# Kernel tuning notes

Measured on AMD Instinct MI355X. Metric: run time of the kernel, lower is better.

## Reference

```python
import jax, jax.numpy as jnp
import numpy as np

H = 512          # HIDDEN_DIM
W = 480          # WINDOWWIDTH
NL = 8           # NUMLABELS (output_dim)
STEPS = W // 15  # 32 decoder steps
ATT = W // 16    # 30 attention positions
B = 4            # window batch
L = 12           # per-frame sequence length
D_IN = 32        # input_dim
N = B * W        # 1920 frame sequences


def _lstm(x, Wih, Whh, bih, bhh):
    # x: [T, Bn, Din] -> per-step hidden/cell states [T, Bn, Hd] (torch LSTM gate order i,f,g,o)
    xp = x @ Wih.T + (bih + bhh)
    h0 = jnp.zeros((x.shape[1], Whh.shape[1]), x.dtype)
    def step(carry, xt):
        h, c = carry
        g = xt + h @ Whh.T
        i, f, gg, o = jnp.split(g, 4, axis=-1)
        c = jax.nn.sigmoid(f) * c + jax.nn.sigmoid(i) * jnp.tanh(gg)
        h = jax.nn.sigmoid(o) * jnp.tanh(c)
        return (h, c), (h, c)
    _, (hs, cs) = jax.lax.scan(step, (h0, h0), xp)
    return hs, cs


def _bilstm(x, Wf, Uf, bf, cf, Wb, Ub, bb, cb):
    # x: [Bt, T, D] batch_first; returns ([Bt, T, 2H], h_fwd_final, h_bwd_final)
    xt = jnp.swapaxes(x, 0, 1)
    hf, _ = _lstm(xt, Wf, Uf, bf, cf)
    hb, _ = _lstm(xt[::-1], Wb, Ub, bb, cb)
    out = jnp.concatenate([hf, hb[::-1]], axis=-1)
    return jnp.swapaxes(out, 0, 1), hf[-1], hb[-1]


def _forward(xs, xlengths, enc_Wih, enc_Whh, enc_bih, enc_bhh,
             penc_Wih_f, penc_Whh_f, penc_bih_f, penc_bhh_f,
             penc_Wih_b, penc_Whh_b, penc_bih_b, penc_bhh_b,
             attn_W, attn_b, comb_W, comb_b,
             gru_Wih, gru_Whh, gru_bih, gru_bhh, out_W, out_b):
    # frame-level encoder: packed sequences -> (h, c) at each sequence's true length
    hs, cs = _lstm(xs, enc_Wih, enc_Whh, enc_bih, enc_bhh)   # [L, N, H] each
    idx = xlengths - 1
    ar = jnp.arange(N)
    ctx = jnp.concatenate([hs[idx, ar], cs[idx, ar]], axis=-1)  # [N, 2H]
    ctx = ctx.reshape(B, W // 2, 4 * H)
    # pyramidal BiLSTM stack (dropout is identity at eval)
    out = ctx
    hf = hb = None
    for i in range(4):
        out, hf, hb = _bilstm(ctx, penc_Wih_f[i], penc_Whh_f[i], penc_bih_f[i], penc_bhh_f[i],
                              penc_Wih_b[i], penc_Whh_b[i], penc_bih_b[i], penc_bhh_b[i])
        if i < 3:
            ctx = out.reshape(B, W // (2 ** (i + 2)), 4 * H)
    enc_out = out                                   # [B, ATT, 2H]
    hidden0 = jnp.concatenate([hf, hb], axis=-1)    # [B, 2H]

    def dstep(carry, _):
        inp, h = carry                              # [B, NL], [B, 2H]
        aw = jax.nn.softmax(jnp.concatenate([inp, h], axis=-1) @ attn_W.T + attn_b, axis=-1)
        ctxv = jnp.einsum('bt,btd->bd', aw, enc_out)
        x = jax.nn.relu(jnp.concatenate([inp, ctxv], axis=-1) @ comb_W.T + comb_b)
        # torch GRU cell (gate order r, z, n)
        gi = x @ gru_Wih.T + gru_bih
        gh = h @ gru_Whh.T + gru_bhh
        ir, iz, inn = jnp.split(gi, 3, axis=-1)
        hr, hz, hn = jnp.split(gh, 3, axis=-1)
        r = jax.nn.sigmoid(ir + hr)
        z = jax.nn.sigmoid(iz + hz)
        n = jnp.tanh(inn + r * hn)
        hnew = (1.0 - z) * n + z * h
        logp = jax.nn.log_softmax(hnew @ out_W.T + out_b, axis=-1)
        return (logp, hnew), logp                   # free-running: next input = log-probs

    inp0 = jnp.zeros((B, NL), xs.dtype)
    _, outs = jax.lax.scan(dstep, (inp0, hidden0), None, length=STEPS)  # [STEPS, B, NL]
    return jnp.swapaxes(outs, 0, 1).reshape(B * STEPS, NL)


def setup_inputs() -> dict:
    key = jax.random.key(0)
    ks = jax.random.split(key, 24)
    s = 0.03
    def nrm(k, shape):
        return jax.random.normal(k, shape, dtype=jnp.float32) * s
    return {
        'xs': jax.random.normal(ks[0], (L, N, D_IN), dtype=jnp.float32),
        'xlengths': jax.random.randint(ks[1], (N,), 1, L + 1, dtype=jnp.int32),
        'enc_Wih': nrm(ks[2], (4 * H, D_IN)),
        'enc_Whh': nrm(ks[3], (4 * H, H)),
        'enc_bih': nrm(ks[4], (4 * H,)),
        'enc_bhh': nrm(ks[5], (4 * H,)),
        'penc_Wih_f': nrm(ks[6], (4, 4 * H, 4 * H)),
        'penc_Whh_f': nrm(ks[7], (4, 4 * H, H)),
        'penc_bih_f': nrm(ks[8], (4, 4 * H)),
        'penc_bhh_f': nrm(ks[9], (4, 4 * H)),
        'penc_Wih_b': nrm(ks[10], (4, 4 * H, 4 * H)),
        'penc_Whh_b': nrm(ks[11], (4, 4 * H, H)),
        'penc_bih_b': nrm(ks[12], (4, 4 * H)),
        'penc_bhh_b': nrm(ks[13], (4, 4 * H)),
        'attn_W': nrm(ks[14], (ATT, 2 * H + NL)),
        'attn_b': nrm(ks[15], (ATT,)),
        'comb_W': nrm(ks[16], (H, 2 * H + NL)),
        'comb_b': nrm(ks[17], (H,)),
        'gru_Wih': nrm(ks[18], (3 * 2 * H, H)),
        'gru_Whh': nrm(ks[19], (3 * 2 * H, 2 * H)),
        'gru_bih': nrm(ks[20], (3 * 2 * H,)),
        'gru_bhh': nrm(ks[21], (3 * 2 * H,)),
        'out_W': nrm(ks[22], (NL, 2 * H)),
        'out_b': nrm(ks[23], (NL,)),
    }


def reference(xs, xlengths, enc_Wih, enc_Whh, enc_bih, enc_bhh,
              penc_Wih_f, penc_Whh_f, penc_bih_f, penc_bhh_f,
              penc_Wih_b, penc_Whh_b, penc_bih_b, penc_bhh_b,
              attn_W, attn_b, comb_W, comb_b,
              gru_Wih, gru_Whh, gru_bih, gru_bhh, out_W, out_b):
    return _forward(xs, xlengths, enc_Wih, enc_Whh, enc_bih, enc_bhh,
                    penc_Wih_f, penc_Whh_f, penc_bih_f, penc_bhh_f,
                    penc_Wih_b, penc_Whh_b, penc_bih_b, penc_bhh_b,
                    attn_W, attn_b, comb_W, comb_b,
                    gru_Wih, gru_Whh, gru_bih, gru_bhh, out_W, out_b)
```

## Files before the change

kernel.cpp:

```cpp
#include <hip/hip_runtime.h>
#include <stdint.h>

typedef __attribute__((ext_vector_type(8))) __bf16 bf16x8;
typedef __attribute__((ext_vector_type(4))) float f32x4;
typedef __attribute__((ext_vector_type(4))) unsigned u32x4;

#define DEVI static __device__ __forceinline__
#define SENT 0xFFFFFFFFu

DEVI bf16x8 bzero8(){ bf16x8 r;
#pragma unroll
  for (int i=0;i<8;++i) r[i]=(__bf16)0.0f; return r; }

DEVI bf16x8 ld8(const __bf16* p){ return *(const bf16x8*)p; }
DEVI void st8(__bf16* p, bf16x8 v){ *(bf16x8*)p = v; }

DEVI f32x4 MFMA(bf16x8 a, bf16x8 b, f32x4 c){
  return __builtin_amdgcn_mfma_f32_16x16x32_bf16(a, b, c, 0, 0, 0);
}

DEVI float sigf(float x){ return 1.0f/(1.0f+__expf(-x)); }

DEVI void ast(unsigned* p, unsigned v){ __hip_atomic_store(p, v, __ATOMIC_RELAXED, __HIP_MEMORY_SCOPE_AGENT); }

DEVI unsigned packbf(float a, float b){
  union { __bf16 h[2]; unsigned u; } x; x.h[0]=(__bf16)a; x.h[1]=(__bf16)b; return x.u;
}
DEVI float bflo(unsigned u){ return __builtin_bit_cast(float, u<<16); }
DEVI float bfhi(unsigned u){ return __builtin_bit_cast(float, u & 0xffff0000u); }

DEVI unsigned bad4(u32x4 v){ return (v[0]==SENT)|(v[1]==SENT)|(v[2]==SENT)|(v[3]==SENT); }

DEVI u32x4 ald4(const void* p){
  u32x4 v;
  asm volatile("global_load_dwordx4 %0, %1, off sc0 sc1\n\ts_waitcnt vmcnt(0)"
               : "=&v"(v) : "v"(p) : "memory");
  return v;
}
DEVI u32x4 poll4(const void* p){
  u32x4 v = ald4(p);
  while (bad4(v)){ __builtin_amdgcn_s_sleep(1); v = ald4(p); }
  return v;
}
DEVI void ald4x2(const void* p, u32x4& a, u32x4& b){
  asm volatile("global_load_dwordx4 %0, %2, off sc0 sc1\n\t"
               "global_load_dwordx4 %1, %2, off offset:16 sc0 sc1\n\t"
               "s_waitcnt vmcnt(0)"
               : "=&v"(a), "=&v"(b) : "v"(p) : "memory");
}
DEVI void poll4x2(const void* p, u32x4& a, u32x4& b){
  ald4x2(p, a, b);
  while (bad4(a) | bad4(b)){ __builtin_amdgcn_s_sleep(1); ald4x2(p, a, b); }
}

DEVI void packGroup(const float* W, int Nsrc, int Kreal, int NT, __bf16* dst, long g){
  int kt = (int)(g / (NT*64));
  int rem = (int)(g % (NT*64));
  int nt = rem >> 6, ln = rem & 63;
  int row = nt*16 + (ln & 15);
  int col = kt*32 + ((ln >> 4) << 3);
  bf16x8 v = bzero8();
  if (row < Nsrc){
#pragma unroll
    for (int j=0;j<8;++j){ int c = col + j; if (c < Kreal) v[j] = (__bf16)W[(long)row*Kreal + c]; }
  }
  st8(dst + g*8, v);
}

DEVI void packGroupCat(const float* Wih, const float* Whh, __bf16* dst, long g){
  int kt = (int)(g / (128*64));
  int rem = (int)(g % (128*64));
  int nt = rem >> 6, ln = rem & 63;
  int prow = nt*16 + (ln & 15);
  int src = (prow & 3)*512 + (prow >> 2);
  int col = kt*32 + ((ln >> 4) << 3);
  bf16x8 v;
  if (col < 32){
#pragma unroll
    for (int j=0;j<8;++j) v[j] = (__bf16)Wih[(long)src*32 + col + j];
  } else {
#pragma unroll
    for (int j=0;j<8;++j) v[j] = (__bf16)Whh[(long)src*512 + (col-32) + j];
  }
  st8(dst + g*8, v);
}

__global__ void initK(unsigned* bar, unsigned* hb, unsigned* ctx, unsigned* xb){
  int g = blockIdx.x*256 + threadIdx.x;
  if (g < 3072){ bar[g] = 0u; return; }
  g -= 3072;
  if (g < 6144){ hb[2048 + g] = SENT; return; }
  g -= 6144;
  if (g < 8192){ ctx[g] = SENT; return; }
  g -= 8192;
  if (g < 4096){ xb[g] = SENT; return; }
}

__global__ void packSmallK(const float* __restrict__ xs, const float* __restrict__ eWih,
    const float* __restrict__ eWhh, const float* __restrict__ ebih, const float* __restrict__ ebhh,
    const float* __restrict__ attnW, const float* __restrict__ combW,
    __bf16* __restrict__ xsb, __bf16* __restrict__ wcatp, float* __restrict__ biasc,
    __bf16* __restrict__ attnp, __bf16* __restrict__ combp)
{
  long g = (long)blockIdx.x*blockDim.x + threadIdx.x;
  const long nWcat = 17L*128*64;
  const long nXs   = 92160;
  const long nBias = 2048;
  const long nAttn = 33L*2*64;
  const long nComb = 33L*32*64;
  if (g < nWcat){ packGroupCat(eWih, eWhh, wcatp, g); return; }
  g -= nWcat;
  if (g < nXs){
    const float* s = xs + g*8; bf16x8 v;
#pragma unroll
    for (int j=0;j<8;++j) v[j] = (__bf16)s[j];
    st8(xsb + g*8, v); return;
  }
  g -= nXs;
  if (g < nBias){ int src = ((int)g & 3)*512 + ((int)g >> 2); biasc[g] = ebih[src] + ebhh[src]; return; }
  g -= nBias;
  if (g < nAttn){ packGroup(attnW, 30, 1032, 2, attnp, g); return; }
  g -= nAttn;
  if (g < nComb){ packGroup(combW, 512, 1032, 32, combp, g); return; }
}

__global__ void packPencK(const float* __restrict__ Wf, const float* __restrict__ Wb,
    const float* __restrict__ WhF, const float* __restrict__ WhB,
    const float* __restrict__ bihf, const float* __restrict__ bhhf,
    const float* __restrict__ bihb, const float* __restrict__ bhhb,
    __bf16* __restrict__ pf, __bf16* __restrict__ pb, float* __restrict__ bsum,
    __bf16* __restrict__ pwhh, unsigned* __restrict__ hpy)
{
  long g = (long)blockIdx.x*blockDim.x + threadIdx.x;
  const long nW = 64L*128*64;
  if (g < nW){ packGroup(Wf, 2048, 2048, 128, pf, g); return; }
  g -= nW;
  if (g < nW){ packGroup(Wb, 2048, 2048, 128, pb, g); return; }
  g -= nW;
  if (g < 2048){ bsum[g] = bihf[g] + bhhf[g]; return; }
  g -= 2048;
  if (g < 2048){ bsum[2048+g] = bihb[g] + bhhb[g]; return; }
  g -= 2048;
  if (g < 8192){
    hpy[g] = ((g >> 10) & 3) ? SENT : 0u;
    return;
  }
  g -= 8192;
  if (g < 262144){
    int lane = (int)(g & 63);
    int f    = (int)((g >> 6) & 31);
    int w    = (int)((g >> 11) & 3);
    int slot = (int)((g >> 13) & 15);
    int dir  = (int)((g >> 17) & 1);
    int kt = f >> 1, nt = f & 1;
    int row16 = lane & 15, kch = lane >> 4;
    int srow = w*512 + slot*32 + nt*16 + row16;
    int scol = kt*32 + kch*8;
    const float* W = dir ? WhB : WhF;
    bf16x8 v;
#pragma unroll
    for (int j=0;j<8;++j) v[j] = (__bf16)W[(long)srow*512 + scol + j];
    st8(pwhh + g*8, v);
  }
}

__global__ __launch_bounds__(256, 1) void encStepK(
    const __bf16* __restrict__ xsb,
    __bf16* __restrict__ henc,
    float* __restrict__ cenc,
    const __bf16* __restrict__ wcatp,
    const float* __restrict__ biasc,
    const int* __restrict__ xlen,
    __bf16* __restrict__ ctx,
    int t)
{
  __shared__ float glds[64][260];
  const int tid = threadIdx.x;
  const int w = tid >> 6, ln = tid & 63;
  const int m0 = blockIdx.x * 64;
  const int nb = blockIdx.y;
  f32x4 acc[16];
#pragma unroll
  for (int i=0;i<16;++i) acc[i] = (f32x4){0.f,0.f,0.f,0.f};

  const int arow = m0 + w*16 + (ln & 15);
  const int kc = (ln >> 4) << 3;
  const int ktEnd = (t == 0) ? 1 : 17;
  for (int kt = 0; kt < ktEnd; ++kt){
    bf16x8 a;
    if (kt == 0) a = ld8(xsb + ((long)t*1920 + arow)*32 + kc);
    else         a = ld8(henc + (long)arow*512 + (kt-1)*32 + kc);
    const __bf16* bp = wcatp + (((long)kt*128 + nb*16)*64 + ln)*8;
#pragma unroll
    for (int n2 = 0; n2 < 16; ++n2){
      bf16x8 b = ld8(bp + (long)n2*512);
      acc[n2] = MFMA(a, b, acc[n2]);
    }
  }
  const int r4 = (ln >> 4) << 2;
#pragma unroll
  for (int n2 = 0; n2 < 16; ++n2){
#pragma unroll
    for (int r = 0; r < 4; ++r)
      glds[w*16 + r4 + r][n2*16 + (ln & 15)] = acc[n2][r];
  }
  __syncthreads();
  for (int it = 0; it < 16; ++it){
    int idx = tid + it*256;
    int mrow = idx >> 6, hcl = idx & 63;
    int n = m0 + mrow;
    int hcg = nb*64 + hcl;
    float ig = glds[mrow][hcl*4+0] + biasc[nb*256 + hcl*4+0];
    float fg = glds[mrow][hcl*4+1] + biasc[nb*256 + hcl*4+1];
    float gg = glds[mrow][hcl*4+2] + biasc[nb*256 + hcl*4+2];
    float og = glds[mrow][hcl*4+3] + biasc[nb*256 + hcl*4+3];
    float c_old = (t == 0) ? 0.0f : cenc[(long)n*512 + hcg];
    float cn = sigf(fg)*c_old + sigf(ig)*tanhf(gg);
    float h  = sigf(og)*tanhf(cn);
    cenc[(long)n*512 + hcg] = cn;
    henc[(long)n*512 + hcg] = (__bf16)h;
    if (xlen[n] - 1 == t){
      ctx[(long)n*1024 + hcg]       = (__bf16)h;
      ctx[(long)n*1024 + 512 + hcg] = (__bf16)cn;
    }
  }
}

__global__ __launch_bounds__(1024) void pencInK(
   const __bf16* __restrict__ inb,
   const __bf16* __restrict__ wpf, const __bf16* __restrict__ wpb,
   const float* __restrict__ bsum,
   float* __restrict__ xpf, float* __restrict__ xpb,
   int M)
{
  const int tid = threadIdx.x, ln = tid & 63, wv = tid >> 6;
  const int rg = wv >> 2, cg = wv & 3;
  const int dir = blockIdx.z;
  const int m0 = blockIdx.x*64 + rg*16;
  const int nb = blockIdx.y;
  const __bf16* wp = dir ? wpb : wpf;
  float* xp = dir ? xpb : xpf;
  const float* bs = bsum + dir*2048;
  f32x4 acc[4];
#pragma unroll
  for (int i=0;i<4;++i) acc[i] = (f32x4){0.f,0.f,0.f,0.f};
  const int arow = m0 + (ln & 15);
  const int kc = (ln >> 4) << 3;
  const bool aok = arow < M;
  for (int kt = 0; kt < 64; ++kt){
    bf16x8 a = aok ? ld8(inb + (long)arow*2048 + kt*32 + kc) : bzero8();
    const __bf16* bp = wp + (((long)kt*128 + nb*16 + cg*4)*64 + ln)*8;
#pragma unroll
    for (int q = 0; q < 4; ++q){
      bf16x8 b = ld8(bp + (long)q*512);
      acc[q] = MFMA(a, b, acc[q]);
    }
  }
  const int r4 = (ln >> 4) << 2;
#pragma unroll
  for (int q = 0; q < 4; ++q){
    int col = (nb*16 + cg*4 + q)*16 + (ln & 15);
#pragma unroll
    for (int r = 0; r < 4; ++r){
      int rowo = m0 + r4 + r;
      if (rowo < M) xp[(long)rowo*2048 + col] = acc[q][r] + bs[col];
    }
  }
}

__global__ __launch_bounds__(256, 1) void pyrRecK(
  const __bf16* __restrict__ pwhh,
  const float* __restrict__ xpf, const float* __restrict__ xpb,
  __bf16* __restrict__ hbuf,
  __bf16* __restrict__ outb,
  float* __restrict__ outf,
  float* __restrict__ h0f, __bf16* __restrict__ h0b,
  int T, int isLast)
{
  __shared__ __align__(16) __bf16 hsL[2][4*512];
  __shared__ float glds[4][4][32];
  const int tid = threadIdx.x, ln = tid & 63, w = tid >> 6;
  const int bk = blockIdx.x;
  const int dir = bk >> 4, slot = bk & 15;
  const int hc0 = slot * 32;
  const float* xp = dir ? xpb : xpf;
  unsigned* hbu = (unsigned*)hbuf;

  bf16x8 BF[32];
  {
    const __bf16* wb = pwhh + ((((size_t)(dir*16 + slot)*4 + w)*32)*64 + ln)*8;
#pragma unroll
    for (int f = 0; f < 32; ++f) BF[f] = ld8(wb + (size_t)f*512);
  }

  const int arow = ln & 15;
  const int kc = (ln >> 4) << 3;
  float cv = 0.0f;
  float x0=0.f,x1=0.f,x2=0.f,x3=0.f;
  if (tid < 128){
    int pos0 = dir ? (T-1) : 0;
    const float* xr = xp + ((size_t)((tid>>5)*T + pos0))*2048 + hc0 + (tid & 31);
    x0 = xr[0]; x1 = xr[512]; x2 = xr[1024]; x3 = xr[1536];
  }

  for (int t = 0; t < T; ++t){
    int cur = t & 3, nxt = (t+1) & 3, clr = (t+2) & 3;
    int pos = dir ? (T-1-t) : t;
    {
      u32x4 v = poll4((const char*)hbuf + (size_t)(dir*4 + cur)*4096 + tid*16);
      ((u32x4*)hsL[t & 1])[tid] = v;
    }
    __syncthreads();
    if (tid < 64){
      int b = tid >> 4, i = tid & 15;
      ast(hbu + ((size_t)(dir*4 + clr)*4 + b)*256 + (hc0 >> 1) + i, SENT);
    }
    const __bf16* hs = hsL[t & 1];
    f32x4 a0 = {0.f,0.f,0.f,0.f}, a1 = {0.f,0.f,0.f,0.f};
#pragma unroll
    for (int kt = 0; kt < 16; ++kt){
      bf16x8 a = (arow < 4) ? ld8(hs + arow*512 + kt*32 + kc) : bzero8();
      a0 = MFMA(a, BF[kt*2+0], a0);
      a1 = MFMA(a, BF[kt*2+1], a1);
    }
    float xn0=0.f,xn1=0.f,xn2=0.f,xn3=0.f;
    if (t+1 < T && tid < 128){
      int pos2 = dir ? (T-2-t) : (t+1);
      const float* xr = xp + ((size_t)((tid>>5)*T + pos2))*2048 + hc0 + (tid & 31);
      xn0 = xr[0]; xn1 = xr[512]; xn2 = xr[1024]; xn3 = xr[1536];
    }
    if (ln < 16){
#pragma unroll
      for (int r=0;r<4;++r){ glds[w][r][ln] = a0[r]; glds[w][r][16+ln] = a1[r]; }
    }
    __syncthreads();
    if (tid < 128){
      int b = tid >> 5, hcl = tid & 31, hcg = hc0 + hcl;
      float ig = glds[0][b][hcl] + x0;
      float fg = glds[1][b][hcl] + x1;
      float gg = glds[2][b][hcl] + x2;
      float og = glds[3][b][hcl] + x3;
      cv = sigf(fg)*cv + sigf(ig)*tanhf(gg);
      float h = sigf(og)*tanhf(cv);
      float hn = __shfl_down(h, 1);
      if (!(hcl & 1))
        ast(hbu + ((size_t)(dir*4 + nxt)*4 + b)*256 + (hcg >> 1), packbf(h, hn));
      if (!isLast){
        outb[((long)(b*T + pos))*1024 + dir*512 + hcg] = (__bf16)h;
      } else {
        outf[((long)(b*T + pos))*1024 + dir*512 + hcg] = h;
        if (t == T-1){
          h0f[b*1024 + dir*512 + hcg] = h;
          h0b[b*1024 + dir*512 + hcg] = (__bf16)h;
        }
      }
    }
    x0=xn0; x1=xn1; x2=xn2; x3=xn3;
  }
}

DEVI bf16x8 dfrag(const __bf16* base, const __bf16* inp, int row, int kt, int kc, int stride){
  if (row >= 4) return bzero8();
  int k = kt*32 + kc;
  if (k == 0) return ld8(inp + row*8);
  int off = k - 8;
  return (off < 1024) ? ld8(base + row*stride + off) : bzero8();
}

__global__ __launch_bounds__(256, 1) void decoderK(
  const float* __restrict__ gWih,
  const float* __restrict__ gWhh,
  const float* __restrict__ gbih, const float* __restrict__ gbhh,
  const float* __restrict__ combBias, const float* __restrict__ attnBias,
  const float* __restrict__ outW, const float* __restrict__ outBias,
  const __bf16* __restrict__ attnP, const __bf16* __restrict__ combP,
  const float* __restrict__ encOut,
  const float* __restrict__ h0f,
  __bf16* __restrict__ HB,
  __bf16* __restrict__ CTXB,
  __bf16* __restrict__ XB,
  float* __restrict__ dout)
{
  __shared__ __align__(16) __bf16 giL[96*512];
  __shared__ __align__(16) __bf16 outWL[8*1024];
  __shared__ __align__(16) __bf16 hL[4*1024];
  __shared__ __align__(16) __bf16 ctxvL[4][1056];
  __shared__ __align__(16) __bf16 xL[4][528];
  __shared__ __bf16 encOutL[4][30][32];
  __shared__ __align__(16) __bf16 inpL[32];
  __shared__ float awL[4][30];
  __shared__ float redL[4][8];
  __shared__ float ghL[3][4][32];
  __shared__ float giO[3][4][32];
  __shared__ float combL[4][4][16];
  __shared__ float biL[3][32], bhL[3][32];
  __shared__ float abL[30], cbL[16];

  const int tid = threadIdx.x, ln = tid & 63, w = tid >> 6;
  const int slot = blockIdx.x;
  const int hc0 = slot * 32;
  unsigned* HBu = (unsigned*)HB;
  unsigned* CTXu = (unsigned*)CTXB;
  unsigned* XBu = (unsigned*)XB;

  for (int it = 0; it < 24; ++it){
    int g = it*256 + tid;
    int rho = g >> 6, c8 = g & 63;
    int gate = rho >> 5, r = rho & 31;
    const float* s = gWih + ((long)(gate*1024 + hc0 + r))*512 + c8*8;
    bf16x8 v;
#pragma unroll
    for (int j=0;j<8;++j) v[j] = (__bf16)s[j];
    st8((__bf16*)((char*)giL + ((rho*1024 + c8*16) ^ ((rho & 7) << 4))), v);
  }
  for (int it = 0; it < 32; ++it){
    int g = it*256 + tid;
    outWL[g] = (__bf16)outW[g];
  }
  for (int idx = tid; idx < 3840; idx += 256){
    int b = idx/960, rem = idx%960;
    int t2 = rem >> 5, dl = rem & 31;
    encOutL[b][t2][dl] = (__bf16)encOut[((long)b*30 + t2)*1024 + hc0 + dl];
  }
  if (tid < 96){
    int g2 = tid >> 5, l = tid & 31;
    biL[g2][l] = gbih[g2*1024 + hc0 + l];
    bhL[g2][l] = gbhh[g2*1024 + hc0 + l];
  }
  if (tid < 30) abL[tid] = attnBias[tid];
  if (tid < 16) cbL[tid] = combBias[slot*16 + tid];

  const int row = ln & 15, kc = (ln >> 4) << 3;
  bf16x8 bigF[66];
  if (w == 0){
#pragma unroll
    for (int nt = 0; nt < 2; ++nt)
#pragma unroll
      for (int kt = 0; kt < 33; ++kt)
        bigF[nt*33 + kt] = ld8(attnP + (((size_t)kt*2 + nt)*64 + ln)*8);
  } else {
    int gate = w - 1;
#pragma unroll
    for (int nt = 0; nt < 2; ++nt)
#pragma unroll
      for (int kt = 0; kt < 32; ++kt){
        const float* s = gWhh + ((long)(gate*1024 + hc0 + nt*16 + row))*1024 + kt*32 + kc;
        bf16x8 v;
#pragma unroll
        for (int j=0;j<8;++j) v[j] = (__bf16)s[j];
        bigF[nt*33 + kt] = v;
      }
  }
  const int kt0c = (w == 0) ? 0 : (w*8 + 1);
  const int nkt = (w == 0) ? 9 : 8;
  bf16x8 combF[9];
#pragma unroll
  for (int i = 0; i < 9; ++i)
    combF[i] = (i < nkt) ? ld8(combP + (((size_t)(kt0c+i)*32 + slot)*64 + ln)*8) : bzero8();

  float hold = 0.f;
  if (tid < 128) hold = h0f[(tid>>5)*1024 + hc0 + (tid & 31)];
  __syncthreads();

  for (int s = 0; s <= 32; ++s){
    int cur = s & 3, nxt = (s+1) & 3, clr = (s+2) & 3;
    {
      u32x4 q0, q1;
      poll4x2((const char*)HB + (size_t)cur*8192 + tid*32, q0, q1);
      ((u32x4*)hL)[tid*2]   = q0;
      ((u32x4*)hL)[tid*2+1] = q1;
    }
    __syncthreads();
    if (tid < 64){
      int b = tid >> 4, i = tid & 15;
      ast(HBu  + ((size_t)clr*4 + b)*512 + (hc0 >> 1) + i, SENT);
      ast(CTXu + ((size_t)clr*4 + b)*512 + (hc0 >> 1) + i, SENT);
    }
    if (tid < 32){
      int b = tid >> 3, i = tid & 7;
      ast(XBu + ((size_t)clr*4 + b)*256 + ((slot*16) >> 1) + i, SENT);
    }
    if (s == 0){
      if (tid < 32) inpL[tid] = (__bf16)0.0f;
      __syncthreads();
    } else {
      int o = tid >> 3, sl = tid & 7;
      int b = o >> 3, l = o & 7;
      const unsigned* hlp = (const unsigned*)hL + b*512 + sl*64;
      const unsigned* wlp = (const unsigned*)outWL + l*512 + sl*64;
      float p = 0.f;
      for (int kk = 0; kk < 64; ++kk){
        unsigned u = hlp[kk], t2 = wlp[kk];
        p += bflo(u)*bflo(t2) + bfhi(u)*bfhi(t2);
      }
      p += __shfl_down(p, 4);
      p += __shfl_down(p, 2);
      p += __shfl_down(p, 1);
      if (sl == 0) redL[b][l] = p + outBias[l];
      __syncthreads();
      if (tid < 4){
        float m = redL[tid][0];
        for (int l2=1;l2<8;++l2) m = fmaxf(m, redL[tid][l2]);
        float sum = 0.f;
        for (int l2=0;l2<8;++l2) sum += __expf(redL[tid][l2]-m);
        float lse = m + __logf(sum);
        for (int l2=0;l2<8;++l2){
          float lp = redL[tid][l2] - lse;
          inpL[tid*8 + l2] = (__bf16)lp;
          if (slot == 0) dout[((long)tid*32 + (s-1))*8 + l2] = lp;
        }
      }
      __syncthreads();
    }
    if (s == 32) break;

    if (w == 0){
      f32x4 a0 = {0.f,0.f,0.f,0.f}, a1 = {0.f,0.f,0.f,0.f};
#pragma unroll
      for (int kt = 0; kt < 33; ++kt){
        bf16x8 a = dfrag(hL, inpL, row, kt, kc, 1024);
        a0 = MFMA(a, bigF[kt], a0);
        a1 = MFMA(a, bigF[33+kt], a1);
      }
      if (ln < 16){
#pragma unroll
        for (int r=0;r<4;++r) awL[r][ln] = a0[r] + abL[ln];
        if (16 + ln < 30){
#pragma unroll
          for (int r=0;r<4;++r) awL[r][16+ln] = a1[r] + abL[16+ln];
        }
      }
    } else {
      f32x4 a0 = {0.f,0.f,0.f,0.f}, a1 = {0.f,0.f,0.f,0.f};
#pragma unroll
      for (int kt = 0; kt < 32; ++kt){
        int k = kt*32 + kc;
        bf16x8 a = (row < 4) ? ld8(hL + row*1024 + k) : bzero8();
        a0 = MFMA(a, bigF[kt], a0);
        a1 = MFMA(a, bigF[33+kt], a1);
      }
      if (ln < 16){
        int gate = w - 1;
#pragma unroll
        for (int r=0;r<4;++r){
          ghL[gate][r][ln] = a0[r];
          ghL[gate][r][16+ln] = a1[r];
        }
      }
    }
    __syncthreads();
    if (tid < 4){
      float m = awL[tid][0];
      for (int t2=1;t2<30;++t2) m = fmaxf(m, awL[tid][t2]);
      float sum = 0.f;
      for (int t2=0;t2<30;++t2){ float e = __expf(awL[tid][t2]-m); awL[tid][t2] = e; sum += e; }
      float inv = 1.0f/sum;
      for (int t2=0;t2<30;++t2) awL[tid][t2] *= inv;
    }
    __syncthreads();
    if (tid < 128){
      int b = tid >> 5, dl = tid & 31;
      float sum = 0.f;
      for (int t2=0;t2<30;++t2) sum += awL[b][t2]*(float)encOutL[b][t2][dl];
      float sn = __shfl_down(sum, 1);
      if (!(dl & 1))
        ast(CTXu + ((size_t)cur*4 + b)*512 + ((hc0 + dl) >> 1), packbf(sum, sn));
    }
    {
      u32x4 q0, q1;
      poll4x2((const char*)CTXB + (size_t)cur*8192 + tid*32, q0, q1);
      u32x4* dst = (u32x4*)((char*)&ctxvL[0][0] + (tid>>6)*2112 + (tid&63)*32);
      dst[0] = q0; dst[1] = q1;
    }
    __syncthreads();
    {
      f32x4 acc = {0.f,0.f,0.f,0.f};
#pragma unroll
      for (int i = 0; i < 9; ++i){
        if (i < nkt){
          bf16x8 a = dfrag(&ctxvL[0][0], inpL, row, kt0c+i, kc, 1056);
          acc = MFMA(a, combF[i], acc);
        }
      }
      if (ln < 16){
#pragma unroll
        for (int r=0;r<4;++r) combL[w][r][ln] = acc[r];
      }
    }
    __syncthreads();
    if (tid < 64){
      int r = tid >> 4, l = tid & 15, col = slot*16 + l;
      float x = combL[0][r][l] + combL[1][r][l] + combL[2][r][l] + combL[3][r][l] + cbL[l];
      x = fmaxf(x, 0.0f);
      float xn = __shfl_down(x, 1);
      if (!(l & 1))
        ast(XBu + ((size_t)cur*4 + r)*256 + (col >> 1), packbf(x, xn));
    }
    {
      u32x4 v = poll4((const char*)XB + (size_t)cur*4096 + tid*16);
      u32x4* dst = (u32x4*)((char*)&xL[0][0] + (tid>>6)*1056 + (tid&63)*16);
      dst[0] = v;
    }
    __syncthreads();
    if (w >= 1){
      int gate = w - 1;
      f32x4 a0 = {0.f,0.f,0.f,0.f}, a1 = {0.f,0.f,0.f,0.f};
#pragma unroll
      for (int kt = 0; kt < 16; ++kt){
        int k = kt*32 + kc;
        bf16x8 a = (row < 4) ? ld8(&xL[row][k]) : bzero8();
        int r0 = gate*32 + row, r1 = r0 + 16;
        bf16x8 b0 = ld8((__bf16*)((char*)giL + ((r0*1024 + k*2) ^ ((r0 & 7) << 4))));
        bf16x8 b1 = ld8((__bf16*)((char*)giL + ((r1*1024 + k*2) ^ ((r1 & 7) << 4))));
        a0 = MFMA(a, b0, a0);
        a1 = MFMA(a, b1, a1);
      }
      if (ln < 16){
#pragma unroll
        for (int r=0;r<4;++r){
          giO[gate][r][ln] = a0[r] + biL[gate][ln];
          giO[gate][r][16+ln] = a1[r] + biL[gate][16+ln];
        }
      }
    }
    __syncthreads();
    if (tid < 128){
      int b = tid >> 5, l = tid & 31, hcg = hc0 + l;
      float rr = sigf(giO[0][b][l] + ghL[0][b][l] + bhL[0][l]);
      float zz = sigf(giO[1][b][l] + ghL[1][b][l] + bhL[1][l]);
      float nn = tanhf(giO[2][b][l] + rr*(ghL[2][b][l] + bhL[2][l]));
      float hnew = (1.0f - zz)*nn + zz*hold;
      hold = hnew;
      float h2 = __shfl_down(hnew, 1);
      if (!(l & 1))
        ast(HBu + ((size_t)nxt*4 + b)*512 + (hcg >> 1), packbf(hnew, h2));
    }
  }
}

static const size_t O_BAR   = 0;
static const size_t O_XSB   = 12288;
static const size_t O_WCATP = 1486848;
static const size_t O_BIASC = 3715072;
static const size_t O_HENC  = 3723264;
static const size_t O_PWHH  = 3723264;
static const size_t O_CENC  = 5689344;
static const size_t O_CTX   = 9621504;
static const size_t O_WIHPF = 13553664;
static const size_t O_WIHPB = 21942272;
static const size_t O_BSUM  = 30330880;
static const size_t O_XPF   = 30347264;
static const size_t O_XPB   = 38211584;
static const size_t O_HPYR  = 46075904;
static const size_t O_OUTA  = 46108672;
static const size_t O_OUTB  = 48074752;
static const size_t O_ENCO  = 49057792;
static const size_t O_H0F   = 49549312;
static const size_t O_HB    = 49565696;
static const size_t O_CTXB  = 49598464;
static const size_t O_XB    = 49631232;
static const size_t O_ATTNP = 49647616;
static const size_t O_COMBP = 49715200;

extern "C" void kernel_launch(void* const* d_in, const int* in_sizes, int n_in,
                              void* d_out, int out_size, void* d_ws, size_t ws_size,
                              hipStream_t stream)
{
  const float* xs    = (const float*)d_in[0];
  const int*   xlen  = (const int*)d_in[1];
  const float* eWih  = (const float*)d_in[2];
  const float* eWhh  = (const float*)d_in[3];
  const float* ebih  = (const float*)d_in[4];
  const float* ebhh  = (const float*)d_in[5];
  const float* pWihF = (const float*)d_in[6];
  const float* pWhhF = (const float*)d_in[7];
  const float* pbihF = (const float*)d_in[8];
  const float* pbhhF = (const float*)d_in[9];
  const float* pWihB = (const float*)d_in[10];
  const float* pWhhB = (const float*)d_in[11];
  const float* pbihB = (const float*)d_in[12];
  const float* pbhhB = (const float*)d_in[13];
  const float* attnW = (const float*)d_in[14];
  const float* attnb = (const float*)d_in[15];
  const float* combW = (const float*)d_in[16];
  const float* combb = (const float*)d_in[17];
  const float* gWih  = (const float*)d_in[18];
  const float* gWhh  = (const float*)d_in[19];
  const float* gbih  = (const float*)d_in[20];
  const float* gbhh  = (const float*)d_in[21];
  const float* outW  = (const float*)d_in[22];
  const float* outb  = (const float*)d_in[23];

  char* ws = (char*)d_ws;
  unsigned* BARU  = (unsigned*)(ws + O_BAR);
  __bf16* XSB     = (__bf16*)(ws + O_XSB);
  __bf16* WCATP   = (__bf16*)(ws + O_WCATP);
  float*  BIASC   = (float*)(ws + O_BIASC);
  __bf16* HENC    = (__bf16*)(ws + O_HENC);
  __bf16* PWHH    = (__bf16*)(ws + O_PWHH);
  float*  CENC    = (float*)(ws + O_CENC);
  __bf16* CTX     = (__bf16*)(ws + O_CTX);
  __bf16* WIHPF   = (__bf16*)(ws + O_WIHPF);
  __bf16* WIHPB   = (__bf16*)(ws + O_WIHPB);
  float*  BSUM    = (float*)(ws + O_BSUM);
  float*  XPF     = (float*)(ws + O_XPF);
  float*  XPB     = (float*)(ws + O_XPB);
  __bf16* HPYR    = (__bf16*)(ws + O_HPYR);
  __bf16* OUTA    = (__bf16*)(ws + O_OUTA);
  __bf16* OUTB    = (__bf16*)(ws + O_OUTB);
  float*  ENCO    = (float*)(ws + O_ENCO);
  float*  H0F     = (float*)(ws + O_H0F);
  __bf16* HB      = (__bf16*)(ws + O_HB);
  __bf16* CTXB    = (__bf16*)(ws + O_CTXB);
  __bf16* XB      = (__bf16*)(ws + O_XB);
  __bf16* ATTNP   = (__bf16*)(ws + O_ATTNP);
  __bf16* COMBP   = (__bf16*)(ws + O_COMBP);

  initK<<<84, 256, 0, stream>>>(BARU, (unsigned*)HB, (unsigned*)CTXB, (unsigned*)XB);
  packSmallK<<<1193, 256, 0, stream>>>(xs, eWih, eWhh, ebih, ebhh, attnW, combW,
      XSB, WCATP, BIASC, ATTNP, COMBP);

  for (int t = 0; t < 12; ++t)
    encStepK<<<dim3(30, 8), 256, 0, stream>>>(XSB, HENC, CENC, WCATP, BIASC, xlen, CTX, t);

  const int Ts[4] = {240, 120, 60, 30};
  const __bf16* ins[4] = {CTX, OUTA, OUTB, OUTA};
  __bf16* outs[4] = {OUTA, OUTB, OUTA, OUTB};
  for (int L = 0; L < 4; ++L){
    int T = Ts[L];
    packPencK<<<5168, 256, 0, stream>>>(pWihF + (long)L*2048*2048, pWihB + (long)L*2048*2048,
        pWhhF + (long)L*2048*512, pWhhB + (long)L*2048*512,
        pbihF + L*2048, pbhhF + L*2048, pbihB + L*2048, pbhhB + L*2048,
        WIHPF, WIHPB, BSUM, PWHH, (unsigned*)HPYR);
    int MB = (4*T + 63)/64;
    pencInK<<<dim3(MB, 8, 2), 1024, 0, stream>>>(ins[L], WIHPF, WIHPB, BSUM, XPF, XPB, 4*T);
    pyrRecK<<<32, 256, 0, stream>>>(PWHH, XPF, XPB, HPYR, outs[L], ENCO, H0F, HB,
        T, (L==3) ? 1 : 0);
  }

  decoderK<<<32, 256, 0, stream>>>(gWih, gWhh, gbih, gbhh, combb, attnb, outW, outb,
      ATTNP, COMBP, ENCO, H0F, HB, CTXB, XB, (float*)d_out);
}
```

Before: 2.117 ms.

## Precompute combine-weight times encoder outputs to drop two decoder cross-block exchanges

The combine layer applied to the attention context is rewritten algebraically: a new kernel precomputes M = combW[:,8:] · encOut for every (batch, position) once. Each decoder block can then form the combined input locally as the attention-weighted sum of M rows plus the small label part. This removes the per-step global context and combined-input exchanges, which used atomic sentinel polling between the 32 blocks. It also splits the pyramid recurrent MFMA loop into two independent accumulator chains. The cost is redundant per-block compute of all 512 outputs, plus bf16 rounding of M before the weighted sum.

```diff
diff --git a/kernel.cpp b/kernel.cpp
--- a/kernel.cpp
+++ b/kernel.cpp
@@ -85,29 +85,22 @@
   st8(dst + g*8, v);
 }
 
-__global__ void initK(unsigned* bar, unsigned* hb, unsigned* ctx, unsigned* xb){
+__global__ void initK(unsigned* hb){
   int g = blockIdx.x*256 + threadIdx.x;
-  if (g < 3072){ bar[g] = 0u; return; }
-  g -= 3072;
-  if (g < 6144){ hb[2048 + g] = SENT; return; }
-  g -= 6144;
-  if (g < 8192){ ctx[g] = SENT; return; }
-  g -= 8192;
-  if (g < 4096){ xb[g] = SENT; return; }
+  if (g < 6144) hb[2048 + g] = SENT;
 }
 
 __global__ void packSmallK(const float* __restrict__ xs, const float* __restrict__ eWih,
     const float* __restrict__ eWhh, const float* __restrict__ ebih, const float* __restrict__ ebhh,
-    const float* __restrict__ attnW, const float* __restrict__ combW,
+    const float* __restrict__ attnW,
     __bf16* __restrict__ xsb, __bf16* __restrict__ wcatp, float* __restrict__ biasc,
-    __bf16* __restrict__ attnp, __bf16* __restrict__ combp)
+    __bf16* __restrict__ attnp)
 {
   long g = (long)blockIdx.x*blockDim.x + threadIdx.x;
   const long nWcat = 17L*128*64;
   const long nXs   = 92160;
   const long nBias = 2048;
   const long nAttn = 33L*2*64;
-  const long nComb = 33L*32*64;
   if (g < nWcat){ packGroupCat(eWih, eWhh, wcatp, g); return; }
   g -= nWcat;
   if (g < nXs){
@@ -120,8 +113,6 @@
   if (g < nBias){ int src = ((int)g & 3)*512 + ((int)g >> 2); biasc[g] = ebih[src] + ebhh[src]; return; }
   g -= nBias;
   if (g < nAttn){ packGroup(attnW, 30, 1032, 2, attnp, g); return; }
-  g -= nAttn;
-  if (g < nComb){ packGroup(combW, 512, 1032, 32, combp, g); return; }
 }
 
 __global__ void packPencK(const float* __restrict__ Wf, const float* __restrict__ Wb,
@@ -316,13 +307,17 @@
       ast(hbu + ((size_t)(dir*4 + clr)*4 + b)*256 + (hc0 >> 1) + i, SENT);
     }
     const __bf16* hs = hsL[t & 1];
-    f32x4 a0 = {0.f,0.f,0.f,0.f}, a1 = {0.f,0.f,0.f,0.f};
-#pragma unroll
-    for (int kt = 0; kt < 16; ++kt){
-      bf16x8 a = (arow < 4) ? ld8(hs + arow*512 + kt*32 + kc) : bzero8();
-      a0 = MFMA(a, BF[kt*2+0], a0);
-      a1 = MFMA(a, BF[kt*2+1], a1);
-    }
+    f32x4 a0 = {0.f,0.f,0.f,0.f}, a1 = a0, a2 = a0, a3 = a0;
+#pragma unroll
+    for (int kt = 0; kt < 16; kt += 2){
+      bf16x8 aA = (arow < 4) ? ld8(hs + arow*512 + kt*32 + kc) : bzero8();
+      bf16x8 aB = (arow < 4) ? ld8(hs + arow*512 + (kt+1)*32 + kc) : bzero8();
+      a0 = MFMA(aA, BF[kt*2+0], a0);
+      a1 = MFMA(aA, BF[kt*2+1], a1);
+      a2 = MFMA(aB, BF[kt*2+2], a2);
+      a3 = MFMA(aB, BF[kt*2+3], a3);
+    }
+    a0 += a2; a1 += a3;
     float xn0=0.f,xn1=0.f,xn2=0.f,xn3=0.f;
     if (t+1 < T && tid < 128){
       int pos2 = dir ? (T-2-t) : (t+1);
@@ -359,6 +354,28 @@
   }
 }
 
+__global__ __launch_bounds__(256) void precMK(const float* __restrict__ combW,
+    const float* __restrict__ encOut, __bf16* __restrict__ Mb)
+{
+  __shared__ float eo[1024];
+  int bt = blockIdx.x;
+  int b = bt / 30, t = bt % 30;
+  int tid = threadIdx.x;
+  for (int i = tid; i < 1024; i += 256) eo[i] = encOut[((long)b*30 + t)*1024 + i];
+  __syncthreads();
+#pragma unroll 1
+  for (int cc = 0; cc < 2; ++cc){
+    int c = tid*2 + cc;
+    const f32x4* wr4 = (const f32x4*)(combW + (long)c*1032 + 8);
+    float s = 0.f;
+    for (int d = 0; d < 256; ++d){
+      f32x4 wv = wr4[d];
+      s += wv[0]*eo[d*4] + wv[1]*eo[d*4+1] + wv[2]*eo[d*4+2] + wv[3]*eo[d*4+3];
+    }
+    Mb[((long)b*30 + t)*512 + c] = (__bf16)s;
+  }
+}
+
 DEVI bf16x8 dfrag(const __bf16* base, const __bf16* inp, int row, int kt, int kc, int stride){
   if (row >= 4) return bzero8();
   int k = kt*32 + kc;
@@ -371,37 +388,34 @@
   const float* __restrict__ gWih,
   const float* __restrict__ gWhh,
   const float* __restrict__ gbih, const float* __restrict__ gbhh,
-  const float* __restrict__ combBias, const float* __restrict__ attnBias,
+  const float* __restrict__ combW,
+  const float* __restrict__ combBias,
+  const float* __restrict__ attnBias,
   const float* __restrict__ outW, const float* __restrict__ outBias,
-  const __bf16* __restrict__ attnP, const __bf16* __restrict__ combP,
-  const float* __restrict__ encOut,
+  const __bf16* __restrict__ attnP,
+  const __bf16* __restrict__ Mb,
   const float* __restrict__ h0f,
   __bf16* __restrict__ HB,
-  __bf16* __restrict__ CTXB,
-  __bf16* __restrict__ XB,
   float* __restrict__ dout)
 {
   __shared__ __align__(16) __bf16 giL[96*512];
   __shared__ __align__(16) __bf16 outWL[8*1024];
   __shared__ __align__(16) __bf16 hL[4*1024];
-  __shared__ __align__(16) __bf16 ctxvL[4][1056];
-  __shared__ __align__(16) __bf16 xL[4][528];
-  __shared__ __bf16 encOutL[4][30][32];
+  __shared__ __align__(16) __bf16 xL[4][520];
+  __shared__ __align__(16) __bf16 WcIL[512][8];
   __shared__ __align__(16) __bf16 inpL[32];
-  __shared__ float awL[4][30];
+  __shared__ float awL[4][32];
   __shared__ float redL[4][8];
   __shared__ float ghL[3][4][32];
   __shared__ float giO[3][4][32];
-  __shared__ float combL[4][4][16];
   __shared__ float biL[3][32], bhL[3][32];
-  __shared__ float abL[30], cbL[16];
+  __shared__ float abL[30];
+  __shared__ float cbAllL[512];
 
   const int tid = threadIdx.x, ln = tid & 63, w = tid >> 6;
   const int slot = blockIdx.x;
   const int hc0 = slot * 32;
   unsigned* HBu = (unsigned*)HB;
-  unsigned* CTXu = (unsigned*)CTXB;
-  unsigned* XBu = (unsigned*)XB;
 
   for (int it = 0; it < 24; ++it){
     int g = it*256 + tid;
@@ -417,18 +431,17 @@
     int g = it*256 + tid;
     outWL[g] = (__bf16)outW[g];
   }
-  for (int idx = tid; idx < 3840; idx += 256){
-    int b = idx/960, rem = idx%960;
-    int t2 = rem >> 5, dl = rem & 31;
-    encOutL[b][t2][dl] = (__bf16)encOut[((long)b*30 + t2)*1024 + hc0 + dl];
-  }
+  for (int idx = tid; idx < 4096; idx += 256){
+    int c = idx >> 3, j = idx & 7;
+    WcIL[c][j] = (__bf16)combW[(long)c*1032 + j];
+  }
+  for (int idx = tid; idx < 512; idx += 256) cbAllL[idx] = combBias[idx];
   if (tid < 96){
     int g2 = tid >> 5, l = tid & 31;
     biL[g2][l] = gbih[g2*1024 + hc0 + l];
     bhL[g2][l] = gbhh[g2*1024 + hc0 + l];
   }
   if (tid < 30) abL[tid] = attnBias[tid];
-  if (tid < 16) cbL[tid] = combBias[slot*16 + tid];
 
   const int row = ln & 15, kc = (ln >> 4) << 3;
   bf16x8 bigF[66];
@@ -451,12 +464,6 @@
         bigF[nt*33 + kt] = v;
       }
   }
-  const int kt0c = (w == 0) ? 0 : (w*8 + 1);
-  const int nkt = (w == 0) ? 9 : 8;
-  bf16x8 combF[9];
-#pragma unroll
-  for (int i = 0; i < 9; ++i)
-    combF[i] = (i < nkt) ? ld8(combP + (((size_t)(kt0c+i)*32 + slot)*64 + ln)*8) : bzero8();
 
   float hold = 0.f;
   if (tid < 128) hold = h0f[(tid>>5)*1024 + hc0 + (tid & 31)];
@@ -473,12 +480,7 @@
     __syncthreads();
     if (tid < 64){
       int b = tid >> 4, i = tid & 15;
-      ast(HBu  + ((size_t)clr*4 + b)*512 + (hc0 >> 1) + i, SENT);
-      ast(CTXu + ((size_t)clr*4 + b)*512 + (hc0 >> 1) + i, SENT);
-    }
-    if (tid < 32){
-      int b = tid >> 3, i = tid & 7;
-      ast(XBu + ((size_t)clr*4 + b)*256 + ((slot*16) >> 1) + i, SENT);
+      ast(HBu + ((size_t)clr*4 + b)*512 + (hc0 >> 1) + i, SENT);
     }
     if (s == 0){
       if (tid < 32) inpL[tid] = (__bf16)0.0f;
@@ -558,48 +560,28 @@
       for (int t2=0;t2<30;++t2) awL[tid][t2] *= inv;
     }
     __syncthreads();
-    if (tid < 128){
-      int b = tid >> 5, dl = tid & 31;
-      float sum = 0.f;
-      for (int t2=0;t2<30;++t2) sum += awL[b][t2]*(float)encOutL[b][t2][dl];
-      float sn = __shfl_down(sum, 1);
-      if (!(dl & 1))
-        ast(CTXu + ((size_t)cur*4 + b)*512 + ((hc0 + dl) >> 1), packbf(sum, sn));
-    }
     {
-      u32x4 q0, q1;
-      poll4x2((const char*)CTXB + (size_t)cur*8192 + tid*32, q0, q1);
-      u32x4* dst = (u32x4*)((char*)&ctxvL[0][0] + (tid>>6)*2112 + (tid&63)*32);
-      dst[0] = q0; dst[1] = q1;
-    }
-    __syncthreads();
-    {
-      f32x4 acc = {0.f,0.f,0.f,0.f};
-#pragma unroll
-      for (int i = 0; i < 9; ++i){
-        if (i < nkt){
-          bf16x8 a = dfrag(&ctxvL[0][0], inpL, row, kt0c+i, kc, 1056);
-          acc = MFMA(a, combF[i], acc);
+      int c0 = tid*2;
+#pragma unroll 1
+      for (int b = 0; b < 4; ++b){
+        float z0 = cbAllL[c0], z1 = cbAllL[c0+1];
+#pragma unroll
+        for (int j = 0; j < 8; ++j){
+          float ij = (float)inpL[b*8 + j];
+          z0 += (float)WcIL[c0][j]*ij;
+          z1 += (float)WcIL[c0+1][j]*ij;
         }
-      }
-      if (ln < 16){
-#pragma unroll
-        for (int r=0;r<4;++r) combL[w][r][ln] = acc[r];
-      }
-    }
-    __syncthreads();
-    if (tid < 64){
-      int r = tid >> 4, l = tid & 15, col = slot*16 + l;
-      float x = combL[0][r][l] + combL[1][r][l] + combL[2][r][l] + combL[3][r][l] + cbL[l];
-      x = fmaxf(x, 0.0f);
-      float xn = __shfl_down(x, 1);
-      if (!(l & 1))
-        ast(XBu + ((size_t)cur*4 + r)*256 + (col >> 1), packbf(x, xn));
-    }
-    {
-      u32x4 v = poll4((const char*)XB + (size_t)cur*4096 + tid*16);
-      u32x4* dst = (u32x4*)((char*)&xL[0][0] + (tid>>6)*1056 + (tid&63)*16);
-      dst[0] = v;
+        const unsigned* mp = (const unsigned*)Mb + (((long)b*30)*512 + c0)/2;
+#pragma unroll
+        for (int t2 = 0; t2 < 30; ++t2){
+          unsigned u = mp[t2*256];
+          float a = awL[b][t2];
+          z0 += a*bflo(u);
+          z1 += a*bfhi(u);
+        }
+        xL[b][c0]   = (__bf16)fmaxf(z0, 0.f);
+        xL[b][c0+1] = (__bf16)fmaxf(z1, 0.f);
+      }
     }
     __syncthreads();
     if (w >= 1){
@@ -638,7 +620,6 @@
   }
 }
 
-static const size_t O_BAR   = 0;
 static const size_t O_XSB   = 12288;
 static const size_t O_WCATP = 1486848;
 static const size_t O_BIASC = 3715072;
@@ -657,10 +638,8 @@
 static const size_t O_ENCO  = 49057792;
 static const size_t O_H0F   = 49549312;
 static const size_t O_HB    = 49565696;
-static const size_t O_CTXB  = 49598464;
-static const size_t O_XB    = 49631232;
 static const size_t O_ATTNP = 49647616;
-static const size_t O_COMBP = 49715200;
+static const size_t O_M     = 49782784;
 
 extern "C" void kernel_launch(void* const* d_in, const int* in_sizes, int n_in,
                               void* d_out, int out_size, void* d_ws, size_t ws_size,
@@ -692,7 +671,6 @@
   const float* outb  = (const float*)d_in[23];
 
   char* ws = (char*)d_ws;
-  unsigned* BARU  = (unsigned*)(ws + O_BAR);
   __bf16* XSB     = (__bf16*)(ws + O_XSB);
   __bf16* WCATP   = (__bf16*)(ws + O_WCATP);
   float*  BIASC   = (float*)(ws + O_BIASC);
@@ -711,14 +689,12 @@
   float*  ENCO    = (float*)(ws + O_ENCO);
   float*  H0F     = (float*)(ws + O_H0F);
   __bf16* HB      = (__bf16*)(ws + O_HB);
-  __bf16* CTXB    = (__bf16*)(ws + O_CTXB);
-  __bf16* XB      = (__bf16*)(ws + O_XB);
   __bf16* ATTNP   = (__bf16*)(ws + O_ATTNP);
-  __bf16* COMBP   = (__bf16*)(ws + O_COMBP);
-
-  initK<<<84, 256, 0, stream>>>(BARU, (unsigned*)HB, (unsigned*)CTXB, (unsigned*)XB);
-  packSmallK<<<1193, 256, 0, stream>>>(xs, eWih, eWhh, ebih, ebhh, attnW, combW,
-      XSB, WCATP, BIASC, ATTNP, COMBP);
+  __bf16* MB      = (__bf16*)(ws + O_M);
+
+  initK<<<24, 256, 0, stream>>>((unsigned*)HB);
+  packSmallK<<<929, 256, 0, stream>>>(xs, eWih, eWhh, ebih, ebhh, attnW,
+      XSB, WCATP, BIASC, ATTNP);
 
   for (int t = 0; t < 12; ++t)
     encStepK<<<dim3(30, 8), 256, 0, stream>>>(XSB, HENC, CENC, WCATP, BIASC, xlen, CTX, t);
@@ -732,12 +708,14 @@
         pWhhF + (long)L*2048*512, pWhhB + (long)L*2048*512,
         pbihF + L*2048, pbhhF + L*2048, pbihB + L*2048, pbhhB + L*2048,
         WIHPF, WIHPB, BSUM, PWHH, (unsigned*)HPYR);
-    int MB = (4*T + 63)/64;
-    pencInK<<<dim3(MB, 8, 2), 1024, 0, stream>>>(ins[L], WIHPF, WIHPB, BSUM, XPF, XPB, 4*T);
+    int MBk = (4*T + 63)/64;
+    pencInK<<<dim3(MBk, 8, 2), 1024, 0, stream>>>(ins[L], WIHPF, WIHPB, BSUM, XPF, XPB, 4*T);
     pyrRecK<<<32, 256, 0, stream>>>(PWHH, XPF, XPB, HPYR, outs[L], ENCO, H0F, HB,
         T, (L==3) ? 1 : 0);
   }
 
-  decoderK<<<32, 256, 0, stream>>>(gWih, gWhh, gbih, gbhh, combb, attnb, outW, outb,
-      ATTNP, COMBP, ENCO, H0F, HB, CTXB, XB, (float*)d_out);
-}
+  precMK<<<120, 256, 0, stream>>>(combW, ENCO, MB);
+
+  decoderK<<<32, 256, 0, stream>>>(gWih, gWhh, gbih, gbhh, combW, combb, attnb,
+      outW, outb, ATTNP, MB, H0F, HB, (float*)d_out);
+}
```

Result: slower. 2.211 ms (+4.4%).
